# Kernel optimization log

Hardware: AMD Instinct MI355X
Metric: run time of the kernel (lower is better)

Reference implementation:

```python
import jax, jax.numpy as jnp
import numpy as np

B, D, U = 8192, 1024, 1024

def setup_inputs() -> dict:
    key = jax.random.key(0)
    ks = jax.random.split(key, 20)
    s = 0.02
    inp = {
        'x': jax.random.normal(ks[0], (B, D), jnp.float32),
        'h': jax.random.normal(ks[1], (B, U), jnp.float32),
        'c': jax.random.normal(ks[2], (B, U), jnp.float32),
        'W_i': jax.random.normal(ks[3], (D, U), jnp.float32) * s,
        'W_f': jax.random.normal(ks[4], (D, U), jnp.float32) * s,
        'W_c': jax.random.normal(ks[5], (D, U), jnp.float32) * s,
        'W_o': jax.random.normal(ks[6], (D, U), jnp.float32) * s,
        'U_i': jax.random.normal(ks[7], (U, U), jnp.float32) * s,
        'U_f': jax.random.normal(ks[8], (U, U), jnp.float32) * s,
        'U_c': jax.random.normal(ks[9], (U, U), jnp.float32) * s,
        'U_o': jax.random.normal(ks[10], (U, U), jnp.float32) * s,
        'V_i': jnp.ones((U,), jnp.float32),
        'V_f': jnp.ones((U,), jnp.float32),
        'V_o': jnp.ones((U,), jnp.float32),
        'b_i': jnp.zeros((U,), jnp.float32),
        'b_f': jnp.ones((U,), jnp.float32),
        'b_c': jnp.zeros((U,), jnp.float32),
        'b_o': jnp.zeros((U,), jnp.float32),
    }
    return inp


def reference(x, h, c, W_i, W_f, W_c, W_o, U_i, U_f, U_c, U_o,
              V_i, V_f, V_o, b_i, b_f, b_c, b_o):
    # Fuse the 4 input and 4 recurrent projections into two GEMMs.
    W = jnp.concatenate([W_i, W_f, W_c, W_o], axis=1)   # [D, 4U]
    Uw = jnp.concatenate([U_i, U_f, U_c, U_o], axis=1)  # [U, 4U]
    b = jnp.concatenate([b_i, b_f, b_c, b_o])           # [4U]
    z = x @ W + h @ Uw + b                               # [B, 4U]
    zi, zf, zc, zo = jnp.split(z, 4, axis=1)
    i_t = jax.nn.sigmoid(zi + V_i * c)
    f_t = jax.nn.sigmoid(zf + V_f * c)
    c_tilde = jnp.tanh(zc)
    c_t = f_t * c + i_t * c_tilde
    o_t = jax.nn.sigmoid(zo + V_o * c_t)
    h_t = o_t * jnp.tanh(c_t)
    return (h_t, c_t)
```

## Files before the change

### kernel.cpp

```cpp
#include <hip/hip_runtime.h>
#include <hip/hip_bf16.h>
#include <stdint.h>


#define MM 8192
#define KK 2048
#define NN 4096
#define BM 256
#define BN 256
#define BK 64

typedef __attribute__((ext_vector_type(8))) __bf16 bf16x8;
typedef __attribute__((ext_vector_type(4))) float floatx4;
typedef __attribute__((ext_vector_type(8))) unsigned short ushort8_t;

__device__ __forceinline__ unsigned short f2bf(float f) {
    unsigned int u = __float_as_uint(f);
    u += 0x7FFF + ((u >> 16) & 1);
    return (unsigned short)(u >> 16);
}

__device__ __forceinline__ float fast_sigmoid(float x) {
    return 1.0f / (1.0f + __expf(-x));
}

__device__ __forceinline__ float fast_tanh(float x) {
    return 2.0f / (1.0f + __expf(-2.0f * x)) - 1.0f;
}

__device__ __forceinline__ void async_copy16(const void* g, void* l) {
    __builtin_amdgcn_global_load_lds(
        (const __attribute__((address_space(1))) void*)g,
        (__attribute__((address_space(3))) void*)l,
        16, 0, 0);
}

__global__ void pack_all(const float* __restrict__ x, const float* __restrict__ h,
                         const float* __restrict__ Wi, const float* __restrict__ Wf,
                         const float* __restrict__ Wc, const float* __restrict__ Wo,
                         const float* __restrict__ Ui, const float* __restrict__ Uf,
                         const float* __restrict__ Uc, const float* __restrict__ Uo,
                         unsigned short* __restrict__ A,
                         unsigned short* __restrict__ Wt) {
    __shared__ float tile[64][65];
    int blk = blockIdx.x;
    int tid = threadIdx.x;
    if (blk >= 2048) {
        int t = (blk - 2048) * 256 + tid;
        long base = (long)t * 8;
        int row = (int)(base >> 11);
        int col = (int)(base & 2047);
        const float* src = (col < 1024) ? (x + (long)row * 1024 + col)
                                        : (h + (long)row * 1024 + (col - 1024));
        float4 v0 = *(const float4*)src;
        float4 v1 = *(const float4*)(src + 4);
        ushort8_t o;
        o[0] = f2bf(v0.x); o[1] = f2bf(v0.y); o[2] = f2bf(v0.z); o[3] = f2bf(v0.w);
        o[4] = f2bf(v1.x); o[5] = f2bf(v1.y); o[6] = f2bf(v1.z); o[7] = f2bf(v1.w);
        *(ushort8_t*)(A + base) = o;
        return;
    }
    int z = blk >> 8;
    int rem = blk & 255;
    const float* src;
    switch (z) {
        case 0: src = Wi; break; case 1: src = Wf; break;
        case 2: src = Wc; break; case 3: src = Wo; break;
        case 4: src = Ui; break; case 5: src = Uf; break;
        case 6: src = Uc; break; default: src = Uo; break;
    }
    int g = z & 3;
    int koff = (z >= 4) ? 1024 : 0;
    int d0 = (rem >> 4) * 64;
    int u0 = (rem & 15) * 64;

    int j = tid & 63;
    int ib = tid >> 6;
#pragma unroll
    for (int p = 0; p < 16; ++p) {
        int i = p * 4 + ib;
        tile[i][j] = src[(long)(d0 + i) * 1024 + u0 + j];
    }
    __syncthreads();
    int i2 = (tid & 31) * 2;
    int jb = tid >> 5;
#pragma unroll
    for (int p = 0; p < 8; ++p) {
        int j2 = p * 8 + jb;
        unsigned short a = f2bf(tile[i2][j2]);
        unsigned short b = f2bf(tile[i2 + 1][j2]);
        long orow = (long)((u0 + j2) * 4 + g);
        *(ushort2*)(Wt + orow * 2048 + koff + d0 + i2) = make_ushort2(a, b);
    }
}


#define SBAR()  __builtin_amdgcn_s_barrier()
#define WAITV4() asm volatile("s_waitcnt vmcnt(4)" ::: "memory")
#define WAITV0() asm volatile("s_waitcnt vmcnt(0)" ::: "memory")
#define WAITL0() asm volatile("s_waitcnt lgkmcnt(0)" ::: "memory")

#define STAGE_A(BUF, HALF, KOFF) do { \
    async_copy16(aG + (size_t)((HALF)*128) * 2048 + (KOFF), \
                 smem + (BUF) + (HALF)*16384 + wave*1024); \
    async_copy16(aG + (size_t)((HALF)*128 + 64) * 2048 + (KOFF), \
                 smem + (BUF) + (HALF)*16384 + 8192 + wave*1024); \
  } while (0)
#define STAGE_B(BUF, HALF, KOFF) do { \
    async_copy16(bG + (size_t)((HALF)*128) * 2048 + (KOFF), \
                 smem + (BUF) + 32768 + (HALF)*16384 + wave*1024); \
    async_copy16(bG + (size_t)((HALF)*128 + 64) * 2048 + (KOFF), \
                 smem + (BUF) + 32768 + (HALF)*16384 + 8192 + wave*1024); \
  } while (0)

#define PHASE(BUF, MH, NH, STAGE_STMT, BND) do { \
    bf16x8 af[4][2], bv[2][2]; \
    _Pragma("unroll") \
    for (int mi = 0; mi < 4; ++mi) { \
      const char* ap = aR + (BUF) + ((MH)*128 + mi*16)*128; \
      af[mi][0] = *(const bf16x8*)(ap + sl0); \
      af[mi][1] = *(const bf16x8*)(ap + sl1); \
    } \
    _Pragma("unroll") \
    for (int ni = 0; ni < 2; ++ni) { \
      const char* bp = bR + (BUF) + ((NH)*128 + ni*16)*128; \
      bv[ni][0] = *(const bf16x8*)(bp + sl0); \
      bv[ni][1] = *(const bf16x8*)(bp + sl1); \
    } \
    STAGE_STMT; \
    if (BND) { WAITV4(); } \
    SBAR(); \
    WAITL0(); \
    __builtin_amdgcn_s_setprio(1); \
    _Pragma("unroll") \
    for (int ks = 0; ks < 2; ++ks) \
      _Pragma("unroll") \
      for (int mi = 0; mi < 4; ++mi) \
        _Pragma("unroll") \
        for (int ni = 0; ni < 2; ++ni) \
          acc[MH][mi][NH][ni] = __builtin_amdgcn_mfma_f32_16x16x32_bf16( \
              af[mi][ks], bv[ni][ks], acc[MH][mi][NH][ni], 0, 0, 0); \
    __builtin_amdgcn_s_setprio(0); \
    SBAR(); \
  } while (0)

__global__ __launch_bounds__(512, 2) void lstm_gemm(
    const unsigned short* __restrict__ A,
    const unsigned short* __restrict__ Wt,
    const float* __restrict__ c_in,
    const float* __restrict__ Vi, const float* __restrict__ Vf, const float* __restrict__ Vo,
    const float* __restrict__ bi_p, const float* __restrict__ bf_p,
    const float* __restrict__ bc_p, const float* __restrict__ bo_p,
    float* __restrict__ out) {
    __shared__ __align__(16) char smem[131072];

    int tid = threadIdx.x;
    int wave = tid >> 6;
    int lane = tid & 63;
    int wm = wave >> 2, wn = wave & 3;
    int fr = lane & 15, fc = lane >> 4;
    int m7 = fr & 7;

    int id = blockIdx.x;
    int swz = (id & 7) * 64 + (id >> 3);
    int bx = swz & 31;
    int by = swz >> 5;
    int rm0 = bx * BM;
    int cn0 = by * BN;

    int r_l = lane >> 3;
    int csw = ((lane & 7) ^ r_l) * 8;
    const unsigned short* aG = A  + (size_t)(rm0 + wave * 8 + r_l) * 2048 + csw;
    const unsigned short* bG = Wt + (size_t)(cn0 + wave * 8 + r_l) * 2048 + csw;

    int sl0 = (fc ^ m7) * 16;
    int sl1 = ((4 + fc) ^ m7) * 16;
    const char* aR = smem + (wm * 64 + fr) * 128;
    const char* bR = smem + 32768 + (wn * 32 + fr) * 128;

    floatx4 acc[2][4][2][2];
#pragma unroll
    for (int a0 = 0; a0 < 2; ++a0)
#pragma unroll
      for (int a1 = 0; a1 < 4; ++a1)
#pragma unroll
        for (int a2 = 0; a2 < 2; ++a2)
#pragma unroll
          for (int a3 = 0; a3 < 2; ++a3) acc[a0][a1][a2][a3] = (floatx4)(0.0f);

    STAGE_B(0, 0, 0); STAGE_A(0, 0, 0); STAGE_B(0, 1, 0); STAGE_A(0, 1, 0);
    STAGE_A(65536, 0, 64); STAGE_B(65536, 1, 64);
    WAITV4();
    SBAR();

#pragma unroll 1
    for (int it = 0; it < 16; ++it) {
        int s0 = it * 2;
        int kN1 = ((s0 + 1) & 31) * 64;
        int kN2 = ((s0 + 2) & 31) * 64;
        int kN3 = ((s0 + 3) & 31) * 64;
        PHASE(0,     0, 0, STAGE_A(65536, 1, kN1), 0);
        PHASE(0,     0, 1, STAGE_B(65536, 0, kN1), 0);
        PHASE(0,     1, 1, STAGE_A(0,     0, kN2), 0);
        PHASE(0,     1, 0, STAGE_B(0,     1, kN2), 1);
        PHASE(65536, 0, 0, STAGE_A(0,     1, kN2), 0);
        PHASE(65536, 0, 1, STAGE_B(0,     0, kN2), 0);
        PHASE(65536, 1, 1, STAGE_A(65536, 0, kN3), 0);
        PHASE(65536, 1, 0, STAGE_B(65536, 1, kN3), 1);
    }

    WAITV0();
    SBAR();

    float* zs = (float*)smem;
    int u_b = tid & 63;
    int u_glob = (cn0 >> 2) + u_b;
    float vVi = Vi[u_glob], vVf = Vf[u_glob], vVo = Vo[u_glob];
    float vbi = bi_p[u_glob], vbf = bf_p[u_glob], vbc = bc_p[u_glob], vbo = bo_p[u_glob];
    int zrb = tid >> 6;

#pragma unroll
    for (int mh = 0; mh < 2; ++mh)
#pragma unroll
      for (int mi = 0; mi < 4; ++mi) {
        if (mh | mi) __syncthreads();
#pragma unroll
        for (int nh = 0; nh < 2; ++nh)
#pragma unroll
          for (int ni = 0; ni < 2; ++ni)
#pragma unroll
            for (int r = 0; r < 4; ++r)
              zs[(wm * 16 + fc * 4 + r) * 260 + nh * 128 + wn * 32 + ni * 16 + fr] =
                  acc[mh][mi][nh][ni][r];
        __syncthreads();
#pragma unroll
        for (int t = 0; t < 4; ++t) {
            int zr = t * 8 + zrb;
            floatx4 z4 = *(const floatx4*)(zs + zr * 260 + u_b * 4);
            long row_glob = rm0 + mh * 128 + (zr >> 4) * 64 + mi * 16 + (zr & 15);
            float cv = c_in[row_glob * 1024 + u_glob];
            float i_t = fast_sigmoid(z4[0] + vbi + vVi * cv);
            float f_t = fast_sigmoid(z4[1] + vbf + vVf * cv);
            float ctl = fast_tanh(z4[2] + vbc);
            float c_t = f_t * cv + i_t * ctl;
            float o_t = fast_sigmoid(z4[3] + vbo + vVo * c_t);
            float h_t = o_t * fast_tanh(c_t);
            out[row_glob * 1024 + u_glob] = h_t;
            out[8388608 + row_glob * 1024 + u_glob] = c_t;
        }
      }
}

extern "C" void kernel_launch(void* const* d_in, const int* in_sizes, int n_in,
                              void* d_out, int out_size, void* d_ws, size_t ws_size,
                              hipStream_t stream) {
    const float* x  = (const float*)d_in[0];
    const float* h  = (const float*)d_in[1];
    const float* c  = (const float*)d_in[2];
    const float* Wi = (const float*)d_in[3];
    const float* Wf = (const float*)d_in[4];
    const float* Wc = (const float*)d_in[5];
    const float* Wo = (const float*)d_in[6];
    const float* Ui = (const float*)d_in[7];
    const float* Uf = (const float*)d_in[8];
    const float* Uc = (const float*)d_in[9];
    const float* Uo = (const float*)d_in[10];
    const float* Vi = (const float*)d_in[11];
    const float* Vf = (const float*)d_in[12];
    const float* Vo = (const float*)d_in[13];
    const float* bi = (const float*)d_in[14];
    const float* bf = (const float*)d_in[15];
    const float* bc = (const float*)d_in[16];
    const float* bo = (const float*)d_in[17];

    unsigned short* Abf = (unsigned short*)d_ws;
    unsigned short* Wt  = (unsigned short*)((char*)d_ws + 33554432);

    pack_all<<<dim3(10240), 256, 0, stream>>>(x, h, Wi, Wf, Wc, Wo,
                                              Ui, Uf, Uc, Uo, Abf, Wt);
    lstm_gemm<<<dim3(512), 512, 0, stream>>>(Abf, Wt, c, Vi, Vf, Vo,
                                             bi, bf, bc, bo, (float*)d_out);
}
```

Before: 338.8 us.

## Reuse LDS fragments across quadrants and reorder async staging schedule

Splits the per-phase macro into separate A-load, B-load and MFMA pieces, keeping both B fragment halves in registers. Each loaded A or B fragment then feeds two MFMA quadrants instead of being reloaded every phase, which cuts LDS reads per k-step. The global-to-LDS staging order changes, with one more stage issued in the prologue and the wait threshold raised from vmcnt(4) to vmcnt(6). This uses more registers for the extra B fragments and needs the new stage and wait ordering to stay race-free.

Result: faster. 331.8 us (-2.1%).

```diff
diff --git a/kernel.cpp b/kernel.cpp
--- a/kernel.cpp
+++ b/kernel.cpp
@@ -96,7 +96,7 @@
 
 
 #define SBAR()  __builtin_amdgcn_s_barrier()
-#define WAITV4() asm volatile("s_waitcnt vmcnt(4)" ::: "memory")
+#define WAITV6() asm volatile("s_waitcnt vmcnt(6)" ::: "memory")
 #define WAITV0() asm volatile("s_waitcnt vmcnt(0)" ::: "memory")
 #define WAITL0() asm volatile("s_waitcnt lgkmcnt(0)" ::: "memory")
 
@@ -113,24 +113,23 @@
                  smem + (BUF) + 32768 + (HALF)*16384 + 8192 + wave*1024); \
   } while (0)
 
-#define PHASE(BUF, MH, NH, STAGE_STMT, BND) do { \
-    bf16x8 af[4][2], bv[2][2]; \
+#define LOAD_A(BUF, MH) do { \
     _Pragma("unroll") \
     for (int mi = 0; mi < 4; ++mi) { \
       const char* ap = aR + (BUF) + ((MH)*128 + mi*16)*128; \
       af[mi][0] = *(const bf16x8*)(ap + sl0); \
       af[mi][1] = *(const bf16x8*)(ap + sl1); \
     } \
+  } while (0)
+#define LOAD_B(BUF, NH, DST) do { \
     _Pragma("unroll") \
     for (int ni = 0; ni < 2; ++ni) { \
       const char* bp = bR + (BUF) + ((NH)*128 + ni*16)*128; \
-      bv[ni][0] = *(const bf16x8*)(bp + sl0); \
-      bv[ni][1] = *(const bf16x8*)(bp + sl1); \
+      DST[ni][0] = *(const bf16x8*)(bp + sl0); \
+      DST[ni][1] = *(const bf16x8*)(bp + sl1); \
     } \
-    STAGE_STMT; \
-    if (BND) { WAITV4(); } \
-    SBAR(); \
-    WAITL0(); \
+  } while (0)
+#define MFMA_Q(MH, NH, BV) do { \
     __builtin_amdgcn_s_setprio(1); \
     _Pragma("unroll") \
     for (int ks = 0; ks < 2; ++ks) \
@@ -139,9 +138,8 @@
         _Pragma("unroll") \
         for (int ni = 0; ni < 2; ++ni) \
           acc[MH][mi][NH][ni] = __builtin_amdgcn_mfma_f32_16x16x32_bf16( \
-              af[mi][ks], bv[ni][ks], acc[MH][mi][NH][ni], 0, 0, 0); \
+              af[mi][ks], BV[ni][ks], acc[MH][mi][NH][ni], 0, 0, 0); \
     __builtin_amdgcn_s_setprio(0); \
-    SBAR(); \
   } while (0)
 
 __global__ __launch_bounds__(512, 2) void lstm_gemm(
@@ -188,9 +186,9 @@
 #pragma unroll
           for (int a3 = 0; a3 < 2; ++a3) acc[a0][a1][a2][a3] = (floatx4)(0.0f);
 
-    STAGE_B(0, 0, 0); STAGE_A(0, 0, 0); STAGE_B(0, 1, 0); STAGE_A(0, 1, 0);
-    STAGE_A(65536, 0, 64); STAGE_B(65536, 1, 64);
-    WAITV4();
+    STAGE_A(0, 0, 0); STAGE_B(0, 0, 0); STAGE_B(0, 1, 0); STAGE_A(0, 1, 0);
+    STAGE_A(65536, 0, 64); STAGE_B(65536, 0, 64); STAGE_B(65536, 1, 64);
+    WAITV6();
     SBAR();
 
 #pragma unroll 1
@@ -199,14 +197,49 @@
         int kN1 = ((s0 + 1) & 31) * 64;
         int kN2 = ((s0 + 2) & 31) * 64;
         int kN3 = ((s0 + 3) & 31) * 64;
-        PHASE(0,     0, 0, STAGE_A(65536, 1, kN1), 0);
-        PHASE(0,     0, 1, STAGE_B(65536, 0, kN1), 0);
-        PHASE(0,     1, 1, STAGE_A(0,     0, kN2), 0);
-        PHASE(0,     1, 0, STAGE_B(0,     1, kN2), 1);
-        PHASE(65536, 0, 0, STAGE_A(0,     1, kN2), 0);
-        PHASE(65536, 0, 1, STAGE_B(0,     0, kN2), 0);
-        PHASE(65536, 1, 1, STAGE_A(65536, 0, kN3), 0);
-        PHASE(65536, 1, 0, STAGE_B(65536, 1, kN3), 1);
+        bf16x8 af[4][2], b0[2][2], b1[2][2];
+
+        LOAD_A(0, 0); LOAD_B(0, 0, b0);
+        STAGE_A(65536, 1, kN1);
+        SBAR(); WAITL0();
+        MFMA_Q(0, 0, b0);
+        SBAR();
+        LOAD_B(0, 1, b1);
+        STAGE_A(0, 0, kN2);
+        SBAR(); WAITL0();
+        MFMA_Q(0, 1, b1);
+        SBAR();
+        LOAD_A(0, 1);
+        STAGE_B(0, 0, kN2);
+        SBAR(); WAITL0();
+        MFMA_Q(1, 1, b1);
+        SBAR();
+        STAGE_B(0, 1, kN2);
+        WAITV6();
+        SBAR();
+        MFMA_Q(1, 0, b0);
+        SBAR();
+
+        LOAD_A(65536, 0); LOAD_B(65536, 0, b0);
+        STAGE_A(0, 1, kN2);
+        SBAR(); WAITL0();
+        MFMA_Q(0, 0, b0);
+        SBAR();
+        LOAD_B(65536, 1, b1);
+        STAGE_A(65536, 0, kN3);
+        SBAR(); WAITL0();
+        MFMA_Q(0, 1, b1);
+        SBAR();
+        LOAD_A(65536, 1);
+        STAGE_B(65536, 0, kN3);
+        SBAR(); WAITL0();
+        MFMA_Q(1, 1, b1);
+        SBAR();
+        STAGE_B(65536, 1, kN3);
+        WAITV6();
+        SBAR();
+        MFMA_Q(1, 0, b0);
+        SBAR();
     }
 
     WAITV0();
```
